# Performance work log

Measured on AMD Instinct MI355X. Metric: run time of the kernel, lower is better.

Reference implementation:

```python
import jax, jax.numpy as jnp
import numpy as np

S = 2048
D = 2048
H = 16
HD = D // H
N_CHARS = 1024
LN_EPS = 1e-5


def setup_inputs() -> dict:
    key = jax.random.key(0)
    ks = jax.random.split(key, 12)
    byte_repr = jax.random.normal(ks[0], (S, D), dtype=jnp.float32)
    categories = jax.random.randint(ks[1], (S,), 0, 32, dtype=jnp.int32)
    case = jax.random.randint(ks[2], (S,), 0, 3, dtype=jnp.int32)
    combining = jax.random.randint(ks[3], (S,), 0, 2, dtype=jnp.int32)
    seg_ids = jnp.sort(jax.random.randint(ks[4], (S,), 0, N_CHARS, dtype=jnp.int32))
    sc = 0.02
    cat_emb = jax.random.normal(ks[5], (32, D), dtype=jnp.float32) * sc
    case_emb = jax.random.normal(ks[6], (3, D), dtype=jnp.float32) * sc
    comb_emb = jax.random.normal(ks[7], (2, D), dtype=jnp.float32) * sc
    ln_g = jnp.ones((D,), dtype=jnp.float32)
    ln_b = jnp.zeros((D,), dtype=jnp.float32)
    in_w = jax.random.normal(ks[8], (3 * D, D), dtype=jnp.float32) * (1.0 / np.sqrt(D))
    in_b = jnp.zeros((3 * D,), dtype=jnp.float32)
    out_w = jax.random.normal(ks[9], (D, D), dtype=jnp.float32) * (1.0 / np.sqrt(D))
    out_b = jnp.zeros((D,), dtype=jnp.float32)
    return {
        'byte_repr': byte_repr, 'categories': categories, 'case': case,
        'combining': combining, 'seg_ids': seg_ids,
        'cat_emb': cat_emb, 'case_emb': case_emb, 'comb_emb': comb_emb,
        'ln_g': ln_g, 'ln_b': ln_b,
        'in_w': in_w, 'in_b': in_b, 'out_w': out_w, 'out_b': out_b,
    }


def reference(byte_repr, categories, case, combining, seg_ids,
              cat_emb, case_emb, comb_emb, ln_g, ln_b,
              in_w, in_b, out_w, out_b):
    # fused embedding adds
    x = byte_repr + cat_emb[categories] + case_emb[case] + comb_emb[combining]
    # LayerNorm
    mu = jnp.mean(x, axis=-1, keepdims=True)
    var = jnp.mean(jnp.square(x - mu), axis=-1, keepdims=True)
    xn = (x - mu) * jax.lax.rsqrt(var + LN_EPS) * ln_g + ln_b
    # QKV projection (torch in_proj): [S, 3D]
    qkv = xn @ in_w.T + in_b
    q, k, v = jnp.split(qkv, 3, axis=-1)
    q = q.reshape(S, H, HD).transpose(1, 0, 2)  # [H,S,hd]
    k = k.reshape(S, H, HD).transpose(1, 0, 2)
    v = v.reshape(S, H, HD).transpose(1, 0, 2)
    # additive float mask: 1 inside a character block, 0 elsewhere
    mask = (seg_ids[:, None] == seg_ids[None, :]).astype(x.dtype)
    scores = jnp.einsum('hqd,hkd->hqk', q, k) / np.sqrt(HD) + mask[None]
    attn = jax.nn.softmax(scores, axis=-1)
    o = jnp.einsum('hqk,hkd->hqd', attn, v)  # [H,S,hd]
    o = o.transpose(1, 0, 2).reshape(S, D) @ out_w.T + out_b
    # residual; dropout is identity in eval
    return xn + o
```

## Files before the change

kernel.cpp:

```cpp
#include <hip/hip_runtime.h>
#include <hip/hip_bf16.h>

#define SS 2048
#define DD 2048
#define HH 16
#define HDIM 128

typedef unsigned short u16;
typedef __attribute__((ext_vector_type(8))) short bf16x8;
typedef __attribute__((ext_vector_type(4))) float f32x4;
typedef __attribute__((ext_vector_type(16))) float f32x16;
typedef __attribute__((ext_vector_type(4))) unsigned short u16x4;
typedef __attribute__((ext_vector_type(4))) int i32x4;
typedef __attribute__((ext_vector_type(4))) unsigned int u32x4;

__device__ __forceinline__ u16 f2bf(float f){
  unsigned u = __float_as_uint(f);
  u += 0x7FFFu + ((u >> 16) & 1u);
  return (u16)(u >> 16);
}

__device__ __forceinline__ void gload_lds16(const void* g, void* l){
  __builtin_amdgcn_global_load_lds(
      (const __attribute__((address_space(1))) void*)g,
      (__attribute__((address_space(3))) void*)l, 16, 0, 0);
}

__device__ __forceinline__ f32x4 mfma16(bf16x8 a, bf16x8 b, f32x4 c){
  return __builtin_amdgcn_mfma_f32_16x16x32_bf16(a, b, c, 0, 0, 0);
}
__device__ __forceinline__ f32x16 mfma32(bf16x8 a, bf16x8 b, f32x16 c){
  return __builtin_amdgcn_mfma_f32_32x32x16_bf16(a, b, c, 0, 0, 0);
}

__device__ __forceinline__ void barf(){
  asm volatile("" ::: "memory");
  __builtin_amdgcn_s_barrier();
  asm volatile("" ::: "memory");
}
#define VMCNT2() asm volatile("s_waitcnt vmcnt(2)" ::: "memory")

__global__ __launch_bounds__(256) void k_embed_ln(
    const float* __restrict__ br, const int* __restrict__ cat,
    const int* __restrict__ cse, const int* __restrict__ cmb,
    const float* __restrict__ cat_e, const float* __restrict__ case_e,
    const float* __restrict__ comb_e, const float* __restrict__ lg,
    const float* __restrict__ lb, float* __restrict__ xn32, u16* __restrict__ xn16)
{
  const int s = blockIdx.x, t = threadIdx.x;
  const int lane = t & 63, wave = t >> 6;
  const int c0 = cat[s], c1 = cse[s], c2 = cmb[s];
  const f32x4* pb = (const f32x4*)(br + (size_t)s * DD);
  const f32x4* e0 = (const f32x4*)(cat_e + (size_t)c0 * DD);
  const f32x4* e1 = (const f32x4*)(case_e + (size_t)c1 * DD);
  const f32x4* e2 = (const f32x4*)(comb_e + (size_t)c2 * DD);
  f32x4 xa = pb[t] + e0[t] + e1[t] + e2[t];
  f32x4 xb = pb[t+256] + e0[t+256] + e1[t+256] + e2[t+256];
  float s1 = 0.f, s2 = 0.f;
#pragma unroll
  for (int i = 0; i < 4; ++i){ s1 += xa[i] + xb[i]; s2 += xa[i]*xa[i] + xb[i]*xb[i]; }
#pragma unroll
  for (int off = 32; off > 0; off >>= 1){ s1 += __shfl_down(s1, off); s2 += __shfl_down(s2, off); }
  __shared__ float red[8];
  if (lane == 0){ red[wave*2] = s1; red[wave*2+1] = s2; }
  __syncthreads();
  const float t1 = red[0]+red[2]+red[4]+red[6];
  const float t2 = red[1]+red[3]+red[5]+red[7];
  const float mean = t1 * (1.0f/DD);
  const float var  = t2 * (1.0f/DD) - mean*mean;
  const float rstd = rsqrtf(var + 1e-5f);
  const f32x4* g4 = (const f32x4*)lg;
  const f32x4* b4 = (const f32x4*)lb;
  f32x4 ga = g4[t], gb = g4[t+256], ba = b4[t], bb = b4[t+256];
  f32x4 ya, yb; u16x4 ha, hb;
#pragma unroll
  for (int i = 0; i < 4; ++i){
    ya[i] = (xa[i]-mean)*rstd*ga[i] + ba[i];
    yb[i] = (xb[i]-mean)*rstd*gb[i] + bb[i];
    ha[i] = f2bf(ya[i]); hb[i] = f2bf(yb[i]);
  }
  ((f32x4*)(xn32 + (size_t)s*DD))[t]     = ya;
  ((f32x4*)(xn32 + (size_t)s*DD))[t+256] = yb;
  ((u16x4*)(xn16 + (size_t)s*DD))[t]     = ha;
  ((u16x4*)(xn16 + (size_t)s*DD))[t+256] = hb;
}

__global__ __launch_bounds__(256) void k_f32_to_bf16(
    const float* __restrict__ in, u16* __restrict__ out, int n4)
{
  int i = blockIdx.x * blockDim.x + threadIdx.x;
  const int stride = gridDim.x * blockDim.x;
  for (; i < n4; i += stride){
    f32x4 v = ((const f32x4*)in)[i];
    u16x4 h;
#pragma unroll
    for (int j = 0; j < 4; ++j) h[j] = f2bf(v[j]);
    ((u16x4*)out)[i] = h;
  }
}

__global__ __launch_bounds__(512) void k_gemm_qkv(
    const u16* __restrict__ A, const u16* __restrict__ B, const float* __restrict__ bias,
    u16* __restrict__ qws, u16* __restrict__ kws, u16* __restrict__ vtws)
{
  __shared__ __align__(16) u16 lds[2][4][128*64];
  const int bid = blockIdx.x;
  const int wg = (bid & 7)*24 + (bid >> 3);
  const int bm = wg & 7, bn = wg >> 3;
  const int t = threadIdx.x, lane = t & 63, wid = t >> 6;
  const int wm = wid >> 2, wn = wid & 3;
  const int r16 = lane & 15, g = lane >> 4;
  const u16* Ab = A + (size_t)bm*256*DD;
  const u16* Bb = B + (size_t)bn*256*DD;

  f32x4 acc[8][4] = {};

  auto stage_half = [&](int buf, int kt, int hh){
    const u16* src = (hh < 2) ? Ab : Bb;
    const int rbase = (hh & 1) * 128;
    u16* dst = (u16*)&lds[buf][hh][0];
#pragma unroll
    for (int i = 0; i < 2; ++i){
      const int ci = i*512 + t;
      const int row = ci >> 3, slot = ci & 7;
      gload_lds16(src + (size_t)(rbase + row)*DD + kt*64 + ((slot ^ (row & 7))*8),
                  dst + ci*8);
    }
  };
  auto frag = [&](const u16* half, int row, int k32) -> bf16x8 {
    return *(const bf16x8*)((const char*)half + row*128 + (((k32*4 + g) ^ (row & 7))*16));
  };

  stage_half(0, 0, 0); stage_half(0, 0, 1); stage_half(0, 0, 2); stage_half(0, 0, 3);
  stage_half(1, 1, 0);
  VMCNT2();
  barf();

  const int rB0 = (wn & 1)*64 + r16;
  for (int kt = 0; kt < 32; ++kt){
    const int cur = kt & 1;
    const u16* bufA = &lds[cur][wm][0];
    const u16* bufB = &lds[cur][2 + (wn >> 1)][0];
    bf16x8 a0[4][2], a1[4][2], b0[2][2], b1[2][2];
#pragma unroll
    for (int i = 0; i < 4; ++i){
      a0[i][0] = frag(bufA, i*16 + r16, 0);
      a0[i][1] = frag(bufA, i*16 + r16, 1);
    }
#pragma unroll
    for (int j = 0; j < 2; ++j){
      b0[j][0] = frag(bufB, rB0 + j*16, 0);
      b0[j][1] = frag(bufB, rB0 + j*16, 1);
    }
    if (kt + 1 < 32) stage_half(cur^1, kt+1, 1);
    barf();
    __builtin_amdgcn_s_setprio(1);
#pragma unroll
    for (int k = 0; k < 2; ++k)
#pragma unroll
      for (int i = 0; i < 4; ++i)
#pragma unroll
        for (int j = 0; j < 2; ++j)
          acc[i][j] = mfma16(a0[i][k], b0[j][k], acc[i][j]);
    __builtin_amdgcn_s_setprio(0);
    barf();
#pragma unroll
    for (int j = 0; j < 2; ++j){
      b1[j][0] = frag(bufB, rB0 + (2+j)*16, 0);
      b1[j][1] = frag(bufB, rB0 + (2+j)*16, 1);
    }
    if (kt + 1 < 32) stage_half(cur^1, kt+1, 2);
    barf();
    __builtin_amdgcn_s_setprio(1);
#pragma unroll
    for (int k = 0; k < 2; ++k)
#pragma unroll
      for (int i = 0; i < 4; ++i)
#pragma unroll
        for (int j = 0; j < 2; ++j)
          acc[i][2+j] = mfma16(a0[i][k], b1[j][k], acc[i][2+j]);
    __builtin_amdgcn_s_setprio(0);
    barf();
#pragma unroll
    for (int i = 0; i < 4; ++i){
      a1[i][0] = frag(bufA, (4+i)*16 + r16, 0);
      a1[i][1] = frag(bufA, (4+i)*16 + r16, 1);
    }
    if (kt + 1 < 32) stage_half(cur^1, kt+1, 3);
    barf();
    __builtin_amdgcn_s_setprio(1);
#pragma unroll
    for (int k = 0; k < 2; ++k)
#pragma unroll
      for (int i = 0; i < 4; ++i)
#pragma unroll
        for (int j = 0; j < 2; ++j)
          acc[4+i][2+j] = mfma16(a1[i][k], b1[j][k], acc[4+i][2+j]);
    __builtin_amdgcn_s_setprio(0);
    barf();
    if (kt + 2 < 32) stage_half(cur, kt+2, 0);
    barf();
    __builtin_amdgcn_s_setprio(1);
#pragma unroll
    for (int k = 0; k < 2; ++k)
#pragma unroll
      for (int i = 0; i < 4; ++i)
#pragma unroll
        for (int j = 0; j < 2; ++j)
          acc[4+i][j] = mfma16(a1[i][k], b0[j][k], acc[4+i][j]);
    __builtin_amdgcn_s_setprio(0);
    VMCNT2();
    barf();
  }

  const float qscale = 0.08838834764831845f;
  const int colb = bn*256 + wn*64;
  const int rowb = bm*256 + wm*128 + g*4;
#pragma unroll
  for (int n = 0; n < 4; ++n){
    const int col = colb + n*16 + r16;
    const int which = col >> 11;
    const int h = (col >> 7) & 15;
    const int hd = col & 127;
    const float bi = bias[col];
#pragma unroll
    for (int m = 0; m < 8; ++m){
      const int row0 = rowb + m*16;
      if (which == 0){
#pragma unroll
        for (int r = 0; r < 4; ++r)
          qws[((size_t)h*SS + row0 + r)*HDIM + hd] = f2bf((acc[m][n][r] + bi)*qscale);
      } else if (which == 1){
#pragma unroll
        for (int r = 0; r < 4; ++r)
          kws[((size_t)h*SS + row0 + r)*HDIM + hd] = f2bf(acc[m][n][r] + bi);
      } else {
        u16x4 pk;
#pragma unroll
        for (int r = 0; r < 4; ++r) pk[r] = f2bf(acc[m][n][r] + bi);
        *(u16x4*)&vtws[((size_t)h*HDIM + hd)*SS + row0] = pk;
      }
    }
  }
}

__device__ __forceinline__ void gemm_tile_128(
    const u16* A, const u16* B, int K, int bm, int bn,
    u16* lds_a, u16* lds_b, f32x4 acc[4][4])
{
  const int t = threadIdx.x;
  const int lane = t & 63;
  const int wm = (t >> 6) >> 1, wn = (t >> 6) & 1;
  const int g = lane >> 4, r16 = lane & 15;
  const u16* Ab = A + (size_t)bm * 128 * K;
  const u16* Bb = B + (size_t)bn * 128 * K;
  for (int kt = 0; kt < K; kt += 32){
#pragma unroll
    for (int half = 0; half < 2; ++half){
      const int tt = half*256 + t;
      const int row = tt >> 2, col = (tt & 3) * 8;
      gload_lds16(Ab + (size_t)row*K + kt + col, lds_a + tt*8);
      gload_lds16(Bb + (size_t)row*K + kt + col, lds_b + tt*8);
    }
    __syncthreads();
    bf16x8 af[4], bfr[4];
#pragma unroll
    for (int i = 0; i < 4; ++i){
      af[i]  = *(const bf16x8*)(lds_a + (wm*64 + i*16 + r16)*32 + g*8);
      bfr[i] = *(const bf16x8*)(lds_b + (wn*64 + i*16 + r16)*32 + g*8);
    }
#pragma unroll
    for (int a = 0; a < 4; ++a)
#pragma unroll
      for (int b = 0; b < 4; ++b)
        acc[a][b] = mfma16(af[a], bfr[b], acc[a][b]);
    __syncthreads();
  }
}

__global__ __launch_bounds__(256, 2) void k_attn(
    const u16* __restrict__ q, const u16* __restrict__ kk_, const u16* __restrict__ vt,
    const int* __restrict__ seg, u16* __restrict__ o)
{
  __shared__ __align__(16) char smem[65536];
  __shared__ float stats[2][2][32];
  const int bid = blockIdx.x;
  const int xcd = bid & 7, ii = bid >> 3;
  const int h = xcd*2 + (ii >> 5), qb = ii & 31;
  const int t = threadIdx.x, lane = t & 63, w = t >> 6;
  const int hi = lane >> 5, l31 = lane & 31;
  const int p = w >> 1, qt = w & 1;
  const int q0 = qb*64 + qt*32;

  const char* khead  = (const char*)(kk_ + (size_t)h*SS*HDIM);
  const char* vthead = (const char*)(vt  + (size_t)h*HDIM*SS);

  bf16x8 qf[8];
  {
    const u16* qp = q + ((size_t)h*SS + q0 + l31)*HDIM + hi*8;
#pragma unroll
    for (int c = 0; c < 8; ++c) qf[c] = *(const bf16x8*)(qp + c*16);
  }
  const int seg_q = seg[q0 + l31];
  const int swz = l31 & 7;

  f32x16 oacc[4];
#pragma unroll
  for (int dg = 0; dg < 4; ++dg)
#pragma unroll
    for (int r = 0; r < 16; ++r) oacc[dg][r] = 0.f;
  float m = -1e30f, l = 0.f;

  auto stage = [&](int buf, int kb){
#pragma unroll
    for (int i = 0; i < 4; ++i){
      const int ci = i*256 + t;
      const int row = ci >> 4, slot = ci & 15;
      gload_lds16(khead + (size_t)(kb + row)*256 + ((slot ^ (row & 7))*16),
                  smem + buf*16384 + ci*16);
    }
#pragma unroll
    for (int i = 0; i < 4; ++i){
      const int ci = i*256 + t;
      const int row = ci >> 3, slot = ci & 7;
      gload_lds16(vthead + (size_t)row*(SS*2) + (size_t)kb*2 + ((slot ^ (row & 7))*16),
                  smem + 32768 + buf*16384 + ci*16);
    }
  };

  stage(0, 0);
  __syncthreads();

  for (int it = 0; it < 32; ++it){
    const int cur = it & 1;
    if (it < 31) stage(cur^1, (it+1)*64);

    bf16x8 kf[8];
    const char* kl = smem + cur*16384 + (p*32 + l31)*256;
#pragma unroll
    for (int c = 0; c < 8; ++c)
      kf[c] = *(const bf16x8*)(kl + (((2*c + hi) ^ swz)*16));
    const int kb_w = it*64 + p*32;
    i32x4 sg[4];
#pragma unroll
    for (int rq = 0; rq < 4; ++rq) sg[rq] = *(const i32x4*)(seg + kb_w + rq*8 + hi*4);
    bf16x8 vf[4][2];
#pragma unroll
    for (int dg = 0; dg < 4; ++dg){
      const char* vl = smem + 32768 + cur*16384 + (dg*32 + l31)*128;
#pragma unroll
      for (int ks = 0; ks < 2; ++ks)
        vf[dg][ks] = *(const bf16x8*)(vl + (((p*4 + 2*ks + hi) ^ swz)*16));
    }

    f32x16 se, so;
#pragma unroll
    for (int r = 0; r < 16; ++r){ se[r] = 0.f; so[r] = 0.f; }
#pragma unroll
    for (int c = 0; c < 4; ++c){
      se = mfma32(kf[2*c],   qf[2*c],   se);
      so = mfma32(kf[2*c+1], qf[2*c+1], so);
    }
    f32x16 s = se + so;

    float tm = -1e30f;
#pragma unroll
    for (int r = 0; r < 16; ++r){
      const int sk = sg[r>>2][r&3];
      s[r] += (sk == seg_q) ? 1.0f : 0.0f;
      tm = fmaxf(tm, s[r]);
    }
    tm = fmaxf(tm, __shfl_xor(tm, 32));
    if (!__all(tm <= m + 8.0f)){
      const float mn = fmaxf(m, tm);
      const float sc = __expf(m - mn);
      l *= sc;
#pragma unroll
      for (int dg = 0; dg < 4; ++dg)
#pragma unroll
        for (int r = 0; r < 16; ++r) oacc[dg][r] *= sc;
      m = mn;
    }
    float pr[16]; float ts = 0.f;
#pragma unroll
    for (int r = 0; r < 16; ++r){ pr[r] = __expf(s[r] - m); ts += pr[r]; }
    ts += __shfl_xor(ts, 32);
    l += ts;
    unsigned pk_[8];
#pragma unroll
    for (int i = 0; i < 8; ++i)
      pk_[i] = (unsigned)f2bf(pr[2*i]) | ((unsigned)f2bf(pr[2*i+1]) << 16);
    const unsigned x0 = __shfl_xor(hi ? pk_[0] : pk_[2], 32);
    const unsigned x1 = __shfl_xor(hi ? pk_[1] : pk_[3], 32);
    const unsigned x2 = __shfl_xor(hi ? pk_[4] : pk_[6], 32);
    const unsigned x3 = __shfl_xor(hi ? pk_[5] : pk_[7], 32);
    u32x4 f0, f1;
    f0[0] = hi ? x0 : pk_[0]; f0[1] = hi ? x1 : pk_[1];
    f0[2] = hi ? pk_[2] : x0; f0[3] = hi ? pk_[3] : x1;
    f1[0] = hi ? x2 : pk_[4]; f1[1] = hi ? x3 : pk_[5];
    f1[2] = hi ? pk_[6] : x2; f1[3] = hi ? pk_[7] : x3;
    const bf16x8 pf0 = __builtin_bit_cast(bf16x8, f0);
    const bf16x8 pf1 = __builtin_bit_cast(bf16x8, f1);
#pragma unroll
    for (int dg = 0; dg < 4; ++dg){
      oacc[dg] = mfma32(vf[dg][0], pf0, oacc[dg]);
      oacc[dg] = mfma32(vf[dg][1], pf1, oacc[dg]);
    }
    __syncthreads();
  }

  float* ob = (float*)smem;
  if (p == 1){
    if (lane < 32){ stats[qt][0][l31] = m; stats[qt][1][l31] = l; }
#pragma unroll
    for (int dg = 0; dg < 4; ++dg)
#pragma unroll
      for (int rq = 0; rq < 4; ++rq){
        f32x4 v4;
#pragma unroll
        for (int j = 0; j < 4; ++j) v4[j] = oacc[dg][rq*4 + j];
        *(f32x4*)&ob[(qt*32 + l31)*132 + dg*32 + rq*8 + hi*4] = v4;
      }
  }
  __syncthreads();
  if (p == 0){
    const float m1 = stats[qt][0][l31], l1 = stats[qt][1][l31];
    const float mM = fmaxf(m, m1);
    const float c0 = __expf(m - mM), c1 = __expf(m1 - mM);
    const float inv = 1.0f / (c0*l + c1*l1);
#pragma unroll
    for (int dg = 0; dg < 4; ++dg)
#pragma unroll
      for (int rq = 0; rq < 4; ++rq){
        const f32x4 v1 = *(const f32x4*)&ob[(qt*32 + l31)*132 + dg*32 + rq*8 + hi*4];
        u16x4 h4;
#pragma unroll
        for (int j = 0; j < 4; ++j)
          h4[j] = f2bf((c0*oacc[dg][rq*4 + j] + c1*v1[j]) * inv);
        const int d0 = dg*32 + rq*8 + hi*4;
        *(u16x4*)&o[((size_t)(q0 + l31))*DD + h*HDIM + d0] = h4;
      }
  }
}

__global__ __launch_bounds__(256) void k_gemm_out(
    const u16* __restrict__ A, const u16* __restrict__ B, const float* __restrict__ bias,
    const float* __restrict__ xn32, float* __restrict__ out)
{
  __shared__ __align__(16) u16 lds_a[128*32];
  __shared__ __align__(16) u16 lds_b[128*32];
  const int wg = (blockIdx.x & 7)*32 + (blockIdx.x >> 3);
  const int bm = wg & 15, bn = wg >> 4;
  f32x4 acc[4][4] = {};
  gemm_tile_128(A, B, DD, bm, bn, lds_a, lds_b, acc);
  const int t = threadIdx.x, lane = t & 63;
  const int wm = (t >> 6) >> 1, wn = (t >> 6) & 1;
  const int g = lane >> 4, r16 = lane & 15;
#pragma unroll
  for (int a = 0; a < 4; ++a){
#pragma unroll
    for (int b = 0; b < 4; ++b){
      const int n = bn*128 + wn*64 + b*16 + r16;
      const float bi = bias[n];
#pragma unroll
      for (int rr = 0; rr < 4; ++rr){
        const int s = bm*128 + wm*64 + a*16 + g*4 + rr;
        out[(size_t)s*DD + n] = acc[a][b][rr] + bi + xn32[(size_t)s*DD + n];
      }
    }
  }
}

extern "C" void kernel_launch(void* const* d_in, const int* in_sizes, int n_in,
                              void* d_out, int out_size, void* d_ws, size_t ws_size,
                              hipStream_t stream)
{
  (void)in_sizes; (void)n_in; (void)out_size; (void)ws_size;
  const float* br     = (const float*)d_in[0];
  const int*   cat    = (const int*)d_in[1];
  const int*   cse    = (const int*)d_in[2];
  const int*   cmb    = (const int*)d_in[3];
  const int*   seg    = (const int*)d_in[4];
  const float* cat_e  = (const float*)d_in[5];
  const float* case_e = (const float*)d_in[6];
  const float* comb_e = (const float*)d_in[7];
  const float* ln_g   = (const float*)d_in[8];
  const float* ln_b   = (const float*)d_in[9];
  const float* in_w   = (const float*)d_in[10];
  const float* in_b   = (const float*)d_in[11];
  const float* out_w  = (const float*)d_in[12];
  const float* out_b  = (const float*)d_in[13];
  float* out = (float*)d_out;

  char* ws = (char*)d_ws;
  float* xn32  = (float*)(ws);
  u16*   xn16  = (u16*)(ws + 16777216);
  u16*   inw16 = (u16*)(ws + 25165824);
  u16*   outw16= (u16*)(ws + 50331648);
  u16*   qws   = (u16*)(ws + 58720256);
  u16*   kws   = (u16*)(ws + 67108864);
  u16*   vtws  = (u16*)(ws + 75497472);
  u16*   ows   = (u16*)(ws + 83886080);

  k_embed_ln<<<SS, 256, 0, stream>>>(br, cat, cse, cmb, cat_e, case_e, comb_e,
                                     ln_g, ln_b, xn32, xn16);
  k_f32_to_bf16<<<2048, 256, 0, stream>>>(in_w, inw16, 3*DD*DD/4);
  k_f32_to_bf16<<<2048, 256, 0, stream>>>(out_w, outw16, DD*DD/4);
  k_gemm_qkv<<<192, 512, 0, stream>>>(xn16, inw16, in_b, qws, kws, vtws);
  k_attn<<<512, 256, 0, stream>>>(qws, kws, vtws, seg, ows);
  k_gemm_out<<<256, 256, 0, stream>>>(ows, outw16, out_b, xn32, out);
}
```

Before: 309.6 us.

## Rework output GEMM tiling, merge weight conversions, add MFMA priority hints in attention

```diff
diff --git a/kernel.cpp b/kernel.cpp
--- a/kernel.cpp
+++ b/kernel.cpp
@@ -85,17 +85,22 @@
   ((u16x4*)(xn16 + (size_t)s*DD))[t+256] = hb;
 }
 
-__global__ __launch_bounds__(256) void k_f32_to_bf16(
-    const float* __restrict__ in, u16* __restrict__ out, int n4)
+__global__ __launch_bounds__(256) void k_conv2(
+    const float* __restrict__ a, const float* __restrict__ b,
+    u16* __restrict__ oa, u16* __restrict__ ob, int n4a, int n4b)
 {
   int i = blockIdx.x * blockDim.x + threadIdx.x;
   const int stride = gridDim.x * blockDim.x;
-  for (; i < n4; i += stride){
-    f32x4 v = ((const f32x4*)in)[i];
+  const int n = n4a + n4b;
+  for (; i < n; i += stride){
+    f32x4 v;
+    if (i < n4a) v = ((const f32x4*)a)[i];
+    else         v = ((const f32x4*)b)[i - n4a];
     u16x4 h;
 #pragma unroll
     for (int j = 0; j < 4; ++j) h[j] = f2bf(v[j]);
-    ((u16x4*)out)[i] = h;
+    if (i < n4a) ((u16x4*)oa)[i] = h;
+    else         ((u16x4*)ob)[i - n4a] = h;
   }
 }
 
@@ -244,40 +249,6 @@
   }
 }
 
-__device__ __forceinline__ void gemm_tile_128(
-    const u16* A, const u16* B, int K, int bm, int bn,
-    u16* lds_a, u16* lds_b, f32x4 acc[4][4])
-{
-  const int t = threadIdx.x;
-  const int lane = t & 63;
-  const int wm = (t >> 6) >> 1, wn = (t >> 6) & 1;
-  const int g = lane >> 4, r16 = lane & 15;
-  const u16* Ab = A + (size_t)bm * 128 * K;
-  const u16* Bb = B + (size_t)bn * 128 * K;
-  for (int kt = 0; kt < K; kt += 32){
-#pragma unroll
-    for (int half = 0; half < 2; ++half){
-      const int tt = half*256 + t;
-      const int row = tt >> 2, col = (tt & 3) * 8;
-      gload_lds16(Ab + (size_t)row*K + kt + col, lds_a + tt*8);
-      gload_lds16(Bb + (size_t)row*K + kt + col, lds_b + tt*8);
-    }
-    __syncthreads();
-    bf16x8 af[4], bfr[4];
-#pragma unroll
-    for (int i = 0; i < 4; ++i){
-      af[i]  = *(const bf16x8*)(lds_a + (wm*64 + i*16 + r16)*32 + g*8);
-      bfr[i] = *(const bf16x8*)(lds_b + (wn*64 + i*16 + r16)*32 + g*8);
-    }
-#pragma unroll
-    for (int a = 0; a < 4; ++a)
-#pragma unroll
-      for (int b = 0; b < 4; ++b)
-        acc[a][b] = mfma16(af[a], bfr[b], acc[a][b]);
-    __syncthreads();
-  }
-}
-
 __global__ __launch_bounds__(256, 2) void k_attn(
     const u16* __restrict__ q, const u16* __restrict__ kk_, const u16* __restrict__ vt,
     const int* __restrict__ seg, u16* __restrict__ o)
@@ -356,20 +327,25 @@
     f32x16 se, so;
 #pragma unroll
     for (int r = 0; r < 16; ++r){ se[r] = 0.f; so[r] = 0.f; }
+    __builtin_amdgcn_s_setprio(1);
 #pragma unroll
     for (int c = 0; c < 4; ++c){
       se = mfma32(kf[2*c],   qf[2*c],   se);
       so = mfma32(kf[2*c+1], qf[2*c+1], so);
     }
+    __builtin_amdgcn_s_setprio(0);
     f32x16 s = se + so;
 
-    float tm = -1e30f;
 #pragma unroll
     for (int r = 0; r < 16; ++r){
       const int sk = sg[r>>2][r&3];
       s[r] += (sk == seg_q) ? 1.0f : 0.0f;
-      tm = fmaxf(tm, s[r]);
-    }
+    }
+    float mx0 = fmaxf(fmaxf(s[0],s[1]), fmaxf(s[2],s[3]));
+    float mx1 = fmaxf(fmaxf(s[4],s[5]), fmaxf(s[6],s[7]));
+    float mx2 = fmaxf(fmaxf(s[8],s[9]), fmaxf(s[10],s[11]));
+    float mx3 = fmaxf(fmaxf(s[12],s[13]), fmaxf(s[14],s[15]));
+    float tm = fmaxf(fmaxf(mx0,mx1), fmaxf(mx2,mx3));
     tm = fmaxf(tm, __shfl_xor(tm, 32));
     if (!__all(tm <= m + 8.0f)){
       const float mn = fmaxf(m, tm);
@@ -381,9 +357,14 @@
         for (int r = 0; r < 16; ++r) oacc[dg][r] *= sc;
       m = mn;
     }
-    float pr[16]; float ts = 0.f;
-#pragma unroll
-    for (int r = 0; r < 16; ++r){ pr[r] = __expf(s[r] - m); ts += pr[r]; }
+    float pr[16];
+#pragma unroll
+    for (int r = 0; r < 16; ++r) pr[r] = __expf(s[r] - m);
+    float s0_ = (pr[0]+pr[1]) + (pr[2]+pr[3]);
+    float s1_ = (pr[4]+pr[5]) + (pr[6]+pr[7]);
+    float s2_ = (pr[8]+pr[9]) + (pr[10]+pr[11]);
+    float s3_ = (pr[12]+pr[13]) + (pr[14]+pr[15]);
+    float ts = (s0_+s1_) + (s2_+s3_);
     ts += __shfl_xor(ts, 32);
     l += ts;
     unsigned pk_[8];
@@ -401,11 +382,13 @@
     f1[2] = hi ? pk_[6] : x2; f1[3] = hi ? pk_[7] : x3;
     const bf16x8 pf0 = __builtin_bit_cast(bf16x8, f0);
     const bf16x8 pf1 = __builtin_bit_cast(bf16x8, f1);
+    __builtin_amdgcn_s_setprio(1);
 #pragma unroll
     for (int dg = 0; dg < 4; ++dg){
       oacc[dg] = mfma32(vf[dg][0], pf0, oacc[dg]);
       oacc[dg] = mfma32(vf[dg][1], pf1, oacc[dg]);
     }
+    __builtin_amdgcn_s_setprio(0);
     __syncthreads();
   }
 
@@ -443,29 +426,82 @@
   }
 }
 
-__global__ __launch_bounds__(256) void k_gemm_out(
+__global__ __launch_bounds__(256, 3) void k_gemm_out(
     const u16* __restrict__ A, const u16* __restrict__ B, const float* __restrict__ bias,
     const float* __restrict__ xn32, float* __restrict__ out)
 {
-  __shared__ __align__(16) u16 lds_a[128*32];
-  __shared__ __align__(16) u16 lds_b[128*32];
-  const int wg = (blockIdx.x & 7)*32 + (blockIdx.x >> 3);
-  const int bm = wg & 15, bn = wg >> 4;
-  f32x4 acc[4][4] = {};
-  gemm_tile_128(A, B, DD, bm, bn, lds_a, lds_b, acc);
-  const int t = threadIdx.x, lane = t & 63;
-  const int wm = (t >> 6) >> 1, wn = (t >> 6) & 1;
-  const int g = lane >> 4, r16 = lane & 15;
-#pragma unroll
-  for (int a = 0; a < 4; ++a){
-#pragma unroll
-    for (int b = 0; b < 4; ++b){
-      const int n = bn*128 + wn*64 + b*16 + r16;
+  __shared__ __align__(16) u16 ldsA[2][128*64];
+  __shared__ __align__(16) u16 ldsB[2][64*64];
+  const int bid = blockIdx.x;
+  const int wg = (bid & 7)*64 + (bid >> 3);
+  const int bm = wg >> 5, bn = wg & 31;
+  const int t = threadIdx.x, lane = t & 63, wid = t >> 6;
+  const int wm = wid >> 1, wn = wid & 1;
+  const int r16 = lane & 15, g = lane >> 4;
+  const u16* Ab = A + (size_t)bm*128*DD;
+  const u16* Bb = B + (size_t)bn*64*DD;
+
+  f32x4 acc[4][2] = {};
+
+  auto stage = [&](int buf, int kt){
+#pragma unroll
+    for (int i = 0; i < 4; ++i){
+      const int ci = i*256 + t;
+      const int row = ci >> 3, slot = ci & 7;
+      gload_lds16(Ab + (size_t)row*DD + kt*64 + ((slot ^ (row & 7))*8),
+                  ldsA[buf] + ci*8);
+    }
+#pragma unroll
+    for (int i = 0; i < 2; ++i){
+      const int ci = i*256 + t;
+      const int row = ci >> 3, slot = ci & 7;
+      gload_lds16(Bb + (size_t)row*DD + kt*64 + ((slot ^ (row & 7))*8),
+                  ldsB[buf] + ci*8);
+    }
+  };
+  auto frag = [&](const u16* half, int row, int k32) -> bf16x8 {
+    return *(const bf16x8*)((const char*)half + row*128 + (((k32*4 + g) ^ (row & 7))*16));
+  };
+
+  stage(0, 0);
+  __syncthreads();
+
+  for (int kt = 0; kt < 32; ++kt){
+    const int cur = kt & 1;
+    if (kt + 1 < 32) stage(cur^1, kt+1);
+    bf16x8 af[4][2], bfr[2][2];
+#pragma unroll
+    for (int i = 0; i < 4; ++i){
+      af[i][0] = frag(ldsA[cur], wm*64 + i*16 + r16, 0);
+      af[i][1] = frag(ldsA[cur], wm*64 + i*16 + r16, 1);
+    }
+#pragma unroll
+    for (int j = 0; j < 2; ++j){
+      bfr[j][0] = frag(ldsB[cur], wn*32 + j*16 + r16, 0);
+      bfr[j][1] = frag(ldsB[cur], wn*32 + j*16 + r16, 1);
+    }
+    __builtin_amdgcn_s_setprio(1);
+#pragma unroll
+    for (int k = 0; k < 2; ++k)
+#pragma unroll
+      for (int i = 0; i < 4; ++i)
+#pragma unroll
+        for (int j = 0; j < 2; ++j)
+          acc[i][j] = mfma16(af[i][k], bfr[j][k], acc[i][j]);
+    __builtin_amdgcn_s_setprio(0);
+    __syncthreads();
+  }
+
+#pragma unroll
+  for (int i = 0; i < 4; ++i){
+#pragma unroll
+    for (int j = 0; j < 2; ++j){
+      const int n = bn*64 + wn*32 + j*16 + r16;
       const float bi = bias[n];
 #pragma unroll
-      for (int rr = 0; rr < 4; ++rr){
-        const int s = bm*128 + wm*64 + a*16 + g*4 + rr;
-        out[(size_t)s*DD + n] = acc[a][b][rr] + bi + xn32[(size_t)s*DD + n];
+      for (int r = 0; r < 4; ++r){
+        const int s = bm*128 + wm*64 + i*16 + g*4 + r;
+        out[(size_t)s*DD + n] = acc[i][j][r] + bi + xn32[(size_t)s*DD + n];
       }
     }
   }
@@ -504,9 +540,9 @@
 
   k_embed_ln<<<SS, 256, 0, stream>>>(br, cat, cse, cmb, cat_e, case_e, comb_e,
                                      ln_g, ln_b, xn32, xn16);
-  k_f32_to_bf16<<<2048, 256, 0, stream>>>(in_w, inw16, 3*DD*DD/4);
-  k_f32_to_bf16<<<2048, 256, 0, stream>>>(out_w, outw16, DD*DD/4);
+  k_conv2<<<2048, 256, 0, stream>>>(in_w, out_w, inw16, outw16,
+                                    3*DD*DD/4, DD*DD/4);
   k_gemm_qkv<<<192, 512, 0, stream>>>(xn16, inw16, in_b, qws, kws, vtws);
   k_attn<<<512, 256, 0, stream>>>(qws, kws, vtws, seg, ows);
-  k_gemm_out<<<256, 256, 0, stream>>>(ows, outw16, out_b, xn32, out);
-}
+  k_gemm_out<<<512, 256, 0, stream>>>(ows, outw16, out_b, xn32, out);
+}
```

Result: faster. 299.1 us (-3.4%).
